# Optimization experiments

Measured on AMD Instinct MI355X. Metric: run time of the kernel, lower is better.

## Reference

```python
import jax, jax.numpy as jnp
import numpy as np

B, Q, C, H, W, E, HID_ATT, HID_MLP, NUM_CLASSES, NUM_LABELS = 8, 64, 512, 16, 16, 512, 128, 512, 14, 64


def setup_inputs() -> dict:
    key = jax.random.key(0)
    ks = jax.random.split(key, 16)
    s = 0.02
    return {
        "feature": jax.random.normal(ks[0], (B, C, H, W), jnp.float32),
        "label_ids": jax.random.randint(ks[1], (B, Q), 0, NUM_LABELS),
        "query_table": jax.random.normal(ks[2], (NUM_LABELS, E), jnp.float32) * s,
        "W_film": jax.random.normal(ks[3], (E, 2 * C), jnp.float32) * s,
        "b_film": jnp.zeros((2 * C,), jnp.float32),
        "W_att_h": jax.random.normal(ks[4], (C, HID_ATT), jnp.float32) * s,
        "b_att_h": jnp.zeros((HID_ATT,), jnp.float32),
        "W_att_f": jax.random.normal(ks[5], (HID_ATT, 1), jnp.float32) * s,
        "b_att_f": jnp.zeros((1,), jnp.float32),
        "W_mlp1": jax.random.normal(ks[6], (C, HID_MLP), jnp.float32) * s,
        "b_mlp1": jnp.zeros((HID_MLP,), jnp.float32),
        "W_mlp2": jax.random.normal(ks[7], (HID_MLP, NUM_CLASSES), jnp.float32) * s,
        "b_mlp2": jnp.zeros((NUM_CLASSES,), jnp.float32),
    }


def gelu(x):
    return jax.nn.gelu(x, approximate=False)  # torch default GELU is exact erf


def reference(feature, label_ids, query_table, W_film, b_film, W_att_h, b_att_h,
              W_att_f, b_att_f, W_mlp1, b_mlp1, W_mlp2, b_mlp2):
    # query embedding lookup: (B, Q, E)
    qe = query_table[label_ids]
    # flatten spatial: (B, HW, C)
    f = feature.reshape(feature.shape[0], feature.shape[1], -1).transpose(0, 2, 1)
    # FiLM params from queries: (B, Q, 2C) -> gamma, beta (B, Q, C)
    gb = jnp.einsum("bqe,ec->bqc", qe, W_film) + b_film
    gamma, beta = jnp.split(gb, 2, axis=-1)
    # FiLM-modulated features: (B, Q, HW, C)
    film = f[:, None, :, :] * gamma[:, :, None, :] + beta[:, :, None, :]
    # local attention MLP -> sigmoid gate (B, Q, HW, 1)
    hidden = gelu(jnp.einsum("bqnc,ch->bqnh", film, W_att_h) + b_att_h)
    attn = jax.nn.sigmoid(jnp.einsum("bqnh,ho->bqno", hidden, W_att_f) + b_att_f)
    # weighted sum pool over HW, normalized by attention mass
    pooled = (attn * film).sum(axis=2) / (attn.sum(axis=2) + 1e-8)  # (B, Q, C)
    # classification MLP
    logits = jnp.einsum("bqh,ho->bqo", gelu(jnp.einsum("bqc,ch->bqh", pooled, W_mlp1) + b_mlp1), W_mlp2) + b_mlp2
    return logits  # (B, Q, NUM_CLASSES)
```

## Files before the change

kernel.cpp:

```cpp
#include <hip/hip_runtime.h>
#include <hip/hip_bf16.h>

#define B_    8
#define Q_    64
#define C_    512
#define HW_   256
#define E_    512
#define HATT_ 128
#define HMLP_ 512
#define NCLS_ 14
#define NLAB_ 64

typedef unsigned short u16;
typedef unsigned int   u32;
typedef __attribute__((ext_vector_type(8))) short short8;
typedef __attribute__((ext_vector_type(4))) float f32x4;


__device__ __forceinline__ float gelu_fast(float x) {
    const float ax = fabsf(x);
    const float t  = __builtin_amdgcn_rcpf(1.0f + 0.3275911f * ax);
    const float p  = t * (0.254829592f +
                     t * (-0.284496736f +
                     t * (1.421413741f +
                     t * (-1.453152027f +
                     t * 1.061405429f))));
    const float e  = __expf(-x * x);
    const float er = copysignf(1.0f - p * e, x);
    return 0.5f * x * (1.0f + er);
}
__device__ __forceinline__ float sigmoid_(float x) {
    return 1.0f / (1.0f + __expf(-x));
}
__device__ __forceinline__ u16 f2bf(float x) {
    u32 u = __float_as_uint(x);
    u32 r = (u + 0x7fffu + ((u >> 16) & 1u)) >> 16;
    return (u16)r;
}
__device__ __forceinline__ float bf2f(u16 u) {
    return __uint_as_float(((u32)u) << 16);
}
__device__ __forceinline__ void gl2lds16(const void* gsrc, void* ldsdst) {
    __builtin_amdgcn_global_load_lds(
        (const __attribute__((address_space(1))) u32*)gsrc,
        (__attribute__((address_space(3))) u32*)ldsdst, 16, 0, 0);
}

__global__ __launch_bounds__(256) void prep_gbp(
    const float* __restrict__ qt, const float* __restrict__ W_film,
    float* __restrict__ GBp) {
    __shared__ float qrow[128];
    const int bid = blockIdx.x, t = threadIdx.x;
    const int l = bid >> 2, cq = bid & 3;
    if (t < 128) qrow[t] = qt[l * E_ + cq * 128 + t];
    __syncthreads();
    const float* wp = W_film + (size_t)(cq * 128) * 1024 + t * 4;
    f32x4 a = {0.f, 0.f, 0.f, 0.f};
    #pragma unroll 8
    for (int c = 0; c < 128; ++c) {
        const float4 w = *(const float4*)(wp + (size_t)c * 1024);
        const float q = qrow[c];
        a.x += q * w.x; a.y += q * w.y; a.z += q * w.z; a.w += q * w.w;
    }
    *(f32x4*)&GBp[(size_t)bid * 1024 + t * 4] = a;
}

__global__ __launch_bounds__(256) void prep_rest(
    const float* __restrict__ feature, const float* __restrict__ W_mlp1,
    const int* __restrict__ label_ids, const float* __restrict__ b_film,
    const float* __restrict__ W_att_h, const float* __restrict__ GBp,
    u16* __restrict__ W1bf, u16* __restrict__ fT,
    int* __restrict__ sperm, int* __restrict__ uled,
    int* __restrict__ ustart, int* __restrict__ nuniq,
    float* __restrict__ Gl, float* __restrict__ Bl,
    u16* __restrict__ WgT, float* __restrict__ Dlp) {

    __shared__ __align__(16) char sm[16896];
    const int bid = blockIdx.x, t = threadIdx.x;

    if (bid < 256) {
        float (*tile)[65] = (float(*)[65])sm;
        const int b = bid >> 5, c0 = ((bid >> 2) & 7) * 64, n0 = (bid & 3) * 64;
        const float* fb = feature + (size_t)b * C_ * HW_;
        const int cl = t >> 2, nq = t & 3;
        #pragma unroll
        for (int i = 0; i < 4; ++i) {
            float4 v = *(const float4*)&fb[(c0 + cl) * HW_ + n0 + nq * 16 + i * 4];
            tile[cl][nq * 16 + i * 4 + 0] = v.x;
            tile[cl][nq * 16 + i * 4 + 1] = v.y;
            tile[cl][nq * 16 + i * 4 + 2] = v.z;
            tile[cl][nq * 16 + i * 4 + 3] = v.w;
        }
        __syncthreads();
        const int nl = t >> 2, cqq = t & 3;
        u16 pk[16];
        #pragma unroll
        for (int k = 0; k < 16; ++k) pk[k] = f2bf(tile[cqq * 16 + k][nl]);
        u16* dst = fT + (size_t)(b * HW_ + n0 + nl) * C_ + c0 + cqq * 16;
        *(uint4*)dst       = *(uint4*)pk;
        *(uint4*)(dst + 8) = *(uint4*)(pk + 8);
    } else if (bid < 320) {
        const int b2 = bid - 256;
        #pragma unroll
        for (int k = 0; k < 2; ++k) {
            const int idx = (b2 * 512 + k * 256 + t) * 8;
            float4 v0 = *(const float4*)&W_mlp1[idx];
            float4 v1 = *(const float4*)&W_mlp1[idx + 4];
            u16 pk[8] = {f2bf(v0.x), f2bf(v0.y), f2bf(v0.z), f2bf(v0.w),
                         f2bf(v1.x), f2bf(v1.y), f2bf(v1.z), f2bf(v1.w)};
            *(uint4*)&W1bf[idx] = *(uint4*)pk;
        }
    } else if (bid == 320) {
        int* cnt = (int*)sm;
        int* off = cnt + 512;
        int* aux = off + 512;
        cnt[t] = 0; cnt[t + 256] = 0;
        __syncthreads();
        const int bqa = t, bqb = t + 256;
        const int ka = label_ids[bqa] * 8 + (bqa >> 6);
        const int kb = label_ids[bqb] * 8 + (bqb >> 6);
        atomicAdd(&cnt[ka], 1);
        atomicAdd(&cnt[kb], 1);
        __syncthreads();
        off[t] = cnt[t]; off[t + 256] = cnt[t + 256];
        __syncthreads();
        for (int d = 1; d < 512; d <<= 1) {
            const int i1 = t + 256;
            const int v0 = off[t]  + ((t  >= d) ? off[t  - d] : 0);
            const int v1 = off[i1] + ((i1 >= d) ? off[i1 - d] : 0);
            __syncthreads();
            off[t] = v0; off[i1] = v1;
            __syncthreads();
        }
        aux[t]       = off[t]       - cnt[t];
        aux[t + 256] = off[t + 256] - cnt[t + 256];
        __syncthreads();
        const int pa = atomicAdd(&aux[ka], 1); sperm[pa] = bqa;
        const int pb = atomicAdd(&aux[kb], 1); sperm[pb] = bqb;
        __syncthreads();
        aux[t]       = cnt[t]       ? 1 : 0;
        aux[t + 256] = cnt[t + 256] ? 1 : 0;
        __syncthreads();
        for (int d = 1; d < 512; d <<= 1) {
            const int i1 = t + 256;
            const int v0 = aux[t]  + ((t  >= d) ? aux[t  - d] : 0);
            const int v1 = aux[i1] + ((i1 >= d) ? aux[i1 - d] : 0);
            __syncthreads();
            aux[t] = v0; aux[i1] = v1;
            __syncthreads();
        }
        const int nu = aux[511];
        #pragma unroll
        for (int e = 0; e < 2; ++e) {
            const int k = t + e * 256;
            if (cnt[k]) {
                const int uidx = aux[k] - 1;
                const int st = off[k] - cnt[k];
                ustart[uidx] = st;
                uled[uidx]   = sperm[st] | ((k >> 3) << 16);
            }
        }
        if (t == 0) nuniq[0] = nu;
        for (int j = t; j <= 512; j += 256)
            if (j >= nu) ustart[j] = 512;
    } else {
        float* g_s  = (float*)sm;
        float* b_s  = g_s + 128;
        float* dred = b_s + 128;
        const int wb = bid - 321;
        const int l = wb >> 2, cq = wb & 3;

        if (t < 128) {
            const int c = cq * 128 + t;
            float g = b_film[c], be = b_film[512 + c];
            #pragma unroll
            for (int j = 0; j < 4; ++j) {
                g  += GBp[(size_t)(l * 4 + j) * 1024 + c];
                be += GBp[(size_t)(l * 4 + j) * 1024 + 512 + c];
            }
            g_s[t] = g; b_s[t] = be;
            Gl[l * C_ + c] = g;
            Bl[l * C_ + c] = be;
        }
        __syncthreads();

        const int h = t & 127, ch = t >> 7;
        const int hswz = (h >> 1) & 3;
        float dl = 0.f;
        #pragma unroll
        for (int sl = 0; sl < 2; ++sl) {
            const int ss = cq * 4 + ch * 2 + sl;
            char* dst = (char*)WgT + (size_t)l * 131072 + ss * 8192 + h * 64;
            #pragma unroll
            for (int g = 0; g < 4; ++g) {
                u16 pk[8];
                #pragma unroll
                for (int j = 0; j < 8; ++j) {
                    const int cl = ch * 64 + sl * 32 + g * 8 + j;
                    const float w = W_att_h[(size_t)(cq * 128 + cl) * HATT_ + h];
                    pk[j] = f2bf(g_s[cl] * w);
                    dl += b_s[cl] * w;
                }
                *(uint4*)(dst + ((g ^ hswz) * 16)) = *(uint4*)pk;
            }
        }
        dred[t] = dl;
        __syncthreads();
        if (t < 128)
            Dlp[(size_t)(l * 4 + cq) * 128 + t] = dred[t] + dred[128 + t];
    }
}

__global__ __launch_bounds__(256, 4) void attn_gemm(
    const float* __restrict__ W_att_f, const float* __restrict__ b_att_f,
    const float* __restrict__ b_att_h, const float* __restrict__ Dlp,
    const int*   __restrict__ uled,    const int* __restrict__ nuniq,
    const u16*   __restrict__ WgT,     const u16* __restrict__ fT,
    u16* __restrict__ pPb, float* __restrict__ pA) {

    __shared__ __align__(16) char Ash[2][8192];
    __shared__ __align__(16) char Bsh[2][8192];
    __shared__ float d_s[HATT_];
    __shared__ float wf_s[HATT_];
    __shared__ float attn_part[2][128];
    __shared__ float attn_s[128];

    const int t = threadIdx.x;
    const int idx = blockIdx.x;
    const int u = idx >> 1, nh = idx & 1;
    if (u >= nuniq[0]) return;
    const int ul = uled[u];
    const int bq = ul & 0xffff, l = ul >> 16;
    const int b = bq >> 6;

    if (t < HATT_) {
        d_s[t] = b_att_h[t]
               + Dlp[(size_t)(l * 4 + 0) * 128 + t]
               + Dlp[(size_t)(l * 4 + 1) * 128 + t]
               + Dlp[(size_t)(l * 4 + 2) * 128 + t]
               + Dlp[(size_t)(l * 4 + 3) * 128 + t];
        wf_s[t] = W_att_f[t];
    }

    const u16* fTb = fT + (size_t)b * HW_ * C_ + (size_t)nh * 128 * C_;
    const u16* Wl  = WgT + (size_t)l * 65536;

    const int an0  = t >> 2;
    const int asl0 = (t & 3) ^ ((an0 >> 1) & 3);

    #define STAGE(s_) {                                                       \
        _Pragma("unroll")                                                     \
        for (int it = 0; it < 2; ++it)                                        \
            gl2lds16(fTb + (size_t)(it * 64 + an0) * C_ + (s_) * 32           \
                         + asl0 * 8,                                          \
                     &Ash[(s_) & 1][(it * 256 + t) * 16]);                    \
        _Pragma("unroll")                                                     \
        for (int it = 0; it < 2; ++it)                                        \
            gl2lds16(Wl + (size_t)(s_) * 4096 + (size_t)(it * 256 + t) * 8,   \
                     &Bsh[(s_) & 1][(it * 256 + t) * 16]);                    \
    }

    const int lane = t & 63, w = t >> 6;
    const int wm = w >> 1, wc = w & 1;
    const int lr = lane & 15, lk = lane >> 4;

    const f32x4 zero = {0.f, 0.f, 0.f, 0.f};
    f32x4 acc[4][4];
    #pragma unroll
    for (int mi = 0; mi < 4; ++mi)
        #pragma unroll
        for (int ni = 0; ni < 4; ++ni) acc[mi][ni] = zero;

    STAGE(0);
    STAGE(1);
    asm volatile("s_waitcnt vmcnt(4)" ::: "memory");
    __builtin_amdgcn_sched_barrier(0);
    __builtin_amdgcn_s_barrier();

    #pragma unroll
    for (int s = 0; s < 16; ++s) {
        const char* Ab = Ash[s & 1];
        const char* Bb = Bsh[s & 1];
        short8 af[4], bf[4];
        #pragma unroll
        for (int mi = 0; mi < 4; ++mi) {
            const int nl = wm * 64 + mi * 16 + lr;
            af[mi] = *(const short8*)(Ab + nl * 64 + ((lk ^ ((nl >> 1) & 3)) * 16));
        }
        #pragma unroll
        for (int ni = 0; ni < 4; ++ni) {
            const int h = wc * 64 + ni * 16 + lr;
            bf[ni] = *(const short8*)(Bb + h * 64 + ((lk ^ ((h >> 1) & 3)) * 16));
        }
        asm volatile("s_waitcnt lgkmcnt(0)" ::: "memory");
        __builtin_amdgcn_sched_barrier(0);
        __builtin_amdgcn_s_barrier();
        if (s < 14) STAGE(s + 2);
        #pragma unroll
        for (int mi = 0; mi < 4; ++mi)
            #pragma unroll
            for (int ni = 0; ni < 4; ++ni)
                acc[mi][ni] = __builtin_amdgcn_mfma_f32_16x16x32_bf16(
                    af[mi], bf[ni], acc[mi][ni], 0, 0, 0);
        if (s < 15) {
            __builtin_amdgcn_sched_barrier(0);
            if (s < 14) asm volatile("s_waitcnt vmcnt(4)" ::: "memory");
            else        asm volatile("s_waitcnt vmcnt(0)" ::: "memory");
            __builtin_amdgcn_sched_barrier(0);
            __builtin_amdgcn_s_barrier();
        }
    }

    #pragma unroll
    for (int mi = 0; mi < 4; ++mi) {
        #pragma unroll
        for (int j = 0; j < 4; ++j) {
            float sum = 0.f;
            #pragma unroll
            for (int ni = 0; ni < 4; ++ni) {
                const int h = wc * 64 + ni * 16 + lr;
                sum += gelu_fast(acc[mi][ni][j] + d_s[h]) * wf_s[h];
            }
            sum += __shfl_xor(sum, 1);
            sum += __shfl_xor(sum, 2);
            sum += __shfl_xor(sum, 4);
            sum += __shfl_xor(sum, 8);
            if (lr == 0) attn_part[wc][wm * 64 + mi * 16 + lk * 4 + j] = sum;
        }
    }
    __syncthreads();
    if (t < 128)
        attn_s[t] = sigmoid_(attn_part[0][t] + attn_part[1][t] + b_att_f[0]);
    __syncthreads();
    if (t < 64) {
        float a = attn_s[t] + attn_s[t + 64];
        #pragma unroll
        for (int m = 1; m < 64; m <<= 1) a += __shfl_xor(a, m);
        if (t == 0) pA[u * 2 + nh] = a;
    }

    float* pred = (float*)Ash;
    {
        const int ng = t >> 7, cb = (t & 127) * 4;
        const u16* fp = fTb + cb;
        f32x4 p = zero;
        #pragma unroll 8
        for (int n = ng * 64; n < ng * 64 + 64; ++n) {
            const uint2 v = *(const uint2*)(fp + (size_t)n * C_);
            const float a = attn_s[n];
            p.x += a * __uint_as_float(v.x << 16);
            p.y += a * __uint_as_float(v.x & 0xffff0000u);
            p.z += a * __uint_as_float(v.y << 16);
            p.w += a * __uint_as_float(v.y & 0xffff0000u);
        }
        *(f32x4*)&pred[ng * 512 + cb] = p;
    }
    __syncthreads();
    {
        const int c0 = t * 2;
        const float v0 = pred[c0]     + pred[512 + c0];
        const float v1 = pred[c0 + 1] + pred[512 + c0 + 1];
        u16 pk[2] = {f2bf(v0), f2bf(v1)};
        *(u32*)&pPb[(size_t)(u * 2 + nh) * 512 + c0] = *(u32*)pk;
    }
}

__global__ __launch_bounds__(512) void mlp_head(
    const int*   __restrict__ uled,  const int* __restrict__ ustart,
    const int*   __restrict__ nuniq, const int* __restrict__ sperm,
    const float* __restrict__ Gl, const float* __restrict__ Bl,
    const float* __restrict__ b_mlp1, const float* __restrict__ W_mlp2,
    const float* __restrict__ b_mlp2, const u16* __restrict__ pPb,
    const float* __restrict__ pA,     const u16* __restrict__ W1bf,
    float* __restrict__ out) {

    __shared__ float pooled_s[2][C_];
    __shared__ float zred[2][2][HMLP_];
    __shared__ float z_s[2][HMLP_];
    __shared__ float red_s[32 * NCLS_];

    const int t = threadIdx.x;
    const int u0 = blockIdx.x * 2;
    const int nu = nuniq[0];
    if (u0 >= nu) return;

    {
        const int ui = t >> 8, cc = (t & 255) * 2;
        const int u = u0 + ui;
        if (u < nu) {
            const int l = uled[u] >> 16;
            const float A = pA[u * 2] + pA[u * 2 + 1];
            const float inv = 1.0f / (A + 1e-8f);
            #pragma unroll
            for (int i = 0; i < 2; ++i) {
                const int c = cc + i;
                const float p = bf2f(pPb[(size_t)(u * 2) * 512 + c])
                              + bf2f(pPb[(size_t)(u * 2 + 1) * 512 + c]);
                pooled_s[ui][c] = (Gl[l * C_ + c] * p + Bl[l * C_ + c] * A) * inv;
            }
        } else {
            pooled_s[ui][cc] = 0.f;
            pooled_s[ui][cc + 1] = 0.f;
        }
    }
    __syncthreads();

    {
        const int hp = t & 255, cg = t >> 8;
        float z00 = 0.f, z01 = 0.f, z10 = 0.f, z11 = 0.f;
        const u16* wp = W1bf + hp * 2;
        #pragma unroll 8
        for (int c = cg * 256; c < cg * 256 + 256; ++c) {
            const u32 v = *(const u32*)(wp + (size_t)c * HMLP_);
            const float w0 = __uint_as_float(v << 16);
            const float w1 = __uint_as_float(v & 0xffff0000u);
            const float pa = pooled_s[0][c], pb = pooled_s[1][c];
            z00 += pa * w0; z01 += pa * w1;
            z10 += pb * w0; z11 += pb * w1;
        }
        float2 a0 = {z00, z01}, a1 = {z10, z11};
        *(float2*)&zred[cg][0][hp * 2] = a0;
        *(float2*)&zred[cg][1][hp * 2] = a1;
    }
    __syncthreads();
    {
        const int ui = t >> 8, h2 = (t & 255) * 2;
        #pragma unroll
        for (int i = 0; i < 2; ++i) {
            const int h = h2 + i;
            z_s[ui][h] = gelu_fast(zred[0][ui][h] + zred[1][ui][h] + b_mlp1[h]);
        }
    }
    __syncthreads();

    #pragma unroll
    for (int ui = 0; ui < 2; ++ui) {
        const int u = u0 + ui;
        if (t < 448) {
            const int o = t % 14, seg = t / 14;
            float s = 0.f;
            #pragma unroll
            for (int k = 0; k < 16; ++k) {
                const int h = seg * 16 + k;
                s += z_s[ui][h] * W_mlp2[h * NCLS_ + o];
            }
            red_s[seg * NCLS_ + o] = s;
        }
        __syncthreads();
        if (u < nu && t < NCLS_) {
            float s = b_mlp2[t];
            #pragma unroll
            for (int seg = 0; seg < 32; ++seg) s += red_s[seg * NCLS_ + t];
            const int r0 = ustart[u], r1 = ustart[u + 1];
            for (int r = r0; r < r1; ++r)
                out[sperm[r] * NCLS_ + t] = s;
        }
        __syncthreads();
    }
}

extern "C" void kernel_launch(void* const* d_in, const int* in_sizes, int n_in,
                              void* d_out, int out_size, void* d_ws, size_t ws_size,
                              hipStream_t stream) {
    const float* feature   = (const float*)d_in[0];
    const int*   label_ids = (const int*)  d_in[1];
    const float* qt        = (const float*)d_in[2];
    const float* W_film    = (const float*)d_in[3];
    const float* b_film    = (const float*)d_in[4];
    const float* W_att_h   = (const float*)d_in[5];
    const float* b_att_h   = (const float*)d_in[6];
    const float* W_att_f   = (const float*)d_in[7];
    const float* b_att_f   = (const float*)d_in[8];
    const float* W_mlp1    = (const float*)d_in[9];
    const float* b_mlp1    = (const float*)d_in[10];
    const float* W_mlp2    = (const float*)d_in[11];
    const float* b_mlp2    = (const float*)d_in[12];
    float* out = (float*)d_out;

    char* wsb    = (char*)d_ws;
    float* GBp   = (float*)wsb;
    u16*   pPb   = (u16*)  wsb;
    float* pA    = (float*)(wsb + 1048576);
    int*   sperm = (int*)  (wsb + 1052672);
    int*   uled  = (int*)  (wsb + 1054720);
    int*   ustart= (int*)  (wsb + 1056768);
    int*   nuniq = (int*)  (wsb + 1060864);
    float* Dlp   = (float*)(wsb + 1064960);
    float* Gl    = (float*)(wsb + 1196032);
    float* Bl    = (float*)(wsb + 1327104);
    u16*   W1bf  = (u16*)  (wsb + 1458176);
    u16*   fTp   = (u16*)  (wsb + 1982464);
    u16*   WgT   = (u16*)  (wsb + 4079616);

    hipLaunchKernelGGL(prep_gbp, dim3(256), dim3(256), 0, stream,
                       qt, W_film, GBp);
    hipLaunchKernelGGL(prep_rest, dim3(577), dim3(256), 0, stream,
                       feature, W_mlp1, label_ids, b_film, W_att_h, GBp,
                       W1bf, fTp, sperm, uled, ustart, nuniq, Gl, Bl, WgT, Dlp);
    hipLaunchKernelGGL(attn_gemm, dim3(1024), dim3(256), 0, stream,
                       W_att_f, b_att_f, b_att_h, Dlp, uled, nuniq,
                       WgT, fTp, pPb, pA);
    hipLaunchKernelGGL(mlp_head, dim3(256), dim3(512), 0, stream,
                       uled, ustart, nuniq, sperm, Gl, Bl,
                       b_mlp1, W_mlp2, b_mlp2, pPb, pA, W1bf, out);
}
```

Measured before the change: 64.54 us.

## Fuse attention GEMM and MLP head into one kernel, one block per unique query

Merges the attention GEMM and the classification MLP head into a single kernel. Each 512-thread block now handles all 256 spatial positions of one unique (query, label) pair instead of splitting them across two blocks. This removes one kernel launch and the global round trip of the bf16 partial pooled vectors and attention sums. In exchange, the block count halves and LDS per block grows, which may reduce occupancy. The MLP head no longer shares its W_mlp1 reads across two unique queries per block.

After: 64.04 us. About the same (-0.8%).

```diff
diff --git a/kernel.cpp b/kernel.cpp
--- a/kernel.cpp
+++ b/kernel.cpp
@@ -211,23 +211,30 @@
     }
 }
 
-__global__ __launch_bounds__(256, 4) void attn_gemm(
+__global__ __launch_bounds__(512, 4) void attn_mlp(
     const float* __restrict__ W_att_f, const float* __restrict__ b_att_f,
     const float* __restrict__ b_att_h, const float* __restrict__ Dlp,
     const int*   __restrict__ uled,    const int* __restrict__ nuniq,
+    const int*   __restrict__ ustart,  const int* __restrict__ sperm,
+    const float* __restrict__ Gl,      const float* __restrict__ Bl,
+    const float* __restrict__ b_mlp1,  const float* __restrict__ W_mlp2,
+    const float* __restrict__ b_mlp2,  const u16* __restrict__ W1bf,
     const u16*   __restrict__ WgT,     const u16* __restrict__ fT,
-    u16* __restrict__ pPb, float* __restrict__ pA) {
-
-    __shared__ __align__(16) char Ash[2][8192];
+    float* __restrict__ out) {
+
+    __shared__ __align__(16) char Ash[2][16384];
     __shared__ __align__(16) char Bsh[2][8192];
     __shared__ float d_s[HATT_];
     __shared__ float wf_s[HATT_];
-    __shared__ float attn_part[2][128];
-    __shared__ float attn_s[128];
+    __shared__ float attn_part[2][HW_];
+    __shared__ float attn_s[HW_];
+    __shared__ float pooled_s[C_];
+    __shared__ float z_s[HMLP_];
+    __shared__ float red_s[32 * NCLS_];
+    __shared__ float A_sh;
 
     const int t = threadIdx.x;
-    const int idx = blockIdx.x;
-    const int u = idx >> 1, nh = idx & 1;
+    const int u = blockIdx.x;
     if (u >= nuniq[0]) return;
     const int ul = uled[u];
     const int bq = ul & 0xffff, l = ul >> 16;
@@ -242,7 +249,7 @@
         wf_s[t] = W_att_f[t];
     }
 
-    const u16* fTb = fT + (size_t)b * HW_ * C_ + (size_t)nh * 128 * C_;
+    const u16* fTb = fT + (size_t)b * HW_ * C_;
     const u16* Wl  = WgT + (size_t)l * 65536;
 
     const int an0  = t >> 2;
@@ -251,13 +258,11 @@
     #define STAGE(s_) {                                                       \
         _Pragma("unroll")                                                     \
         for (int it = 0; it < 2; ++it)                                        \
-            gl2lds16(fTb + (size_t)(it * 64 + an0) * C_ + (s_) * 32           \
+            gl2lds16(fTb + (size_t)(it * 128 + an0) * C_ + (s_) * 32          \
                          + asl0 * 8,                                          \
-                     &Ash[(s_) & 1][(it * 256 + t) * 16]);                    \
-        _Pragma("unroll")                                                     \
-        for (int it = 0; it < 2; ++it)                                        \
-            gl2lds16(Wl + (size_t)(s_) * 4096 + (size_t)(it * 256 + t) * 8,   \
-                     &Bsh[(s_) & 1][(it * 256 + t) * 16]);                    \
+                     &Ash[(s_) & 1][(it * 512 + t) * 16]);                    \
+        gl2lds16(Wl + (size_t)(s_) * 4096 + (size_t)t * 8,                    \
+                 &Bsh[(s_) & 1][t * 16]);                                     \
     }
 
     const int lane = t & 63, w = t >> 6;
@@ -273,7 +278,7 @@
 
     STAGE(0);
     STAGE(1);
-    asm volatile("s_waitcnt vmcnt(4)" ::: "memory");
+    asm volatile("s_waitcnt vmcnt(3)" ::: "memory");
     __builtin_amdgcn_sched_barrier(0);
     __builtin_amdgcn_s_barrier();
 
@@ -304,7 +309,7 @@
                     af[mi], bf[ni], acc[mi][ni], 0, 0, 0);
         if (s < 15) {
             __builtin_amdgcn_sched_barrier(0);
-            if (s < 14) asm volatile("s_waitcnt vmcnt(4)" ::: "memory");
+            if (s < 14) asm volatile("s_waitcnt vmcnt(3)" ::: "memory");
             else        asm volatile("s_waitcnt vmcnt(0)" ::: "memory");
             __builtin_amdgcn_sched_barrier(0);
             __builtin_amdgcn_s_barrier();
@@ -329,15 +334,16 @@
         }
     }
     __syncthreads();
-    if (t < 128)
+    if (t < HW_)
         attn_s[t] = sigmoid_(attn_part[0][t] + attn_part[1][t] + b_att_f[0]);
     __syncthreads();
     if (t < 64) {
-        float a = attn_s[t] + attn_s[t + 64];
+        float a = attn_s[t] + attn_s[t + 64] + attn_s[t + 128] + attn_s[t + 192];
         #pragma unroll
         for (int m = 1; m < 64; m <<= 1) a += __shfl_xor(a, m);
-        if (t == 0) pA[u * 2 + nh] = a;
-    }
+        if (t == 0) A_sh = a;
+    }
+    __syncthreads();
 
     float* pred = (float*)Ash;
     {
@@ -357,105 +363,50 @@
     }
     __syncthreads();
     {
-        const int c0 = t * 2;
-        const float v0 = pred[c0]     + pred[512 + c0];
-        const float v1 = pred[c0 + 1] + pred[512 + c0 + 1];
-        u16 pk[2] = {f2bf(v0), f2bf(v1)};
-        *(u32*)&pPb[(size_t)(u * 2 + nh) * 512 + c0] = *(u32*)pk;
-    }
-}
-
-__global__ __launch_bounds__(512) void mlp_head(
-    const int*   __restrict__ uled,  const int* __restrict__ ustart,
-    const int*   __restrict__ nuniq, const int* __restrict__ sperm,
-    const float* __restrict__ Gl, const float* __restrict__ Bl,
-    const float* __restrict__ b_mlp1, const float* __restrict__ W_mlp2,
-    const float* __restrict__ b_mlp2, const u16* __restrict__ pPb,
-    const float* __restrict__ pA,     const u16* __restrict__ W1bf,
-    float* __restrict__ out) {
-
-    __shared__ float pooled_s[2][C_];
-    __shared__ float zred[2][2][HMLP_];
-    __shared__ float z_s[2][HMLP_];
-    __shared__ float red_s[32 * NCLS_];
-
-    const int t = threadIdx.x;
-    const int u0 = blockIdx.x * 2;
-    const int nu = nuniq[0];
-    if (u0 >= nu) return;
-
-    {
-        const int ui = t >> 8, cc = (t & 255) * 2;
-        const int u = u0 + ui;
-        if (u < nu) {
-            const int l = uled[u] >> 16;
-            const float A = pA[u * 2] + pA[u * 2 + 1];
-            const float inv = 1.0f / (A + 1e-8f);
-            #pragma unroll
-            for (int i = 0; i < 2; ++i) {
-                const int c = cc + i;
-                const float p = bf2f(pPb[(size_t)(u * 2) * 512 + c])
-                              + bf2f(pPb[(size_t)(u * 2 + 1) * 512 + c]);
-                pooled_s[ui][c] = (Gl[l * C_ + c] * p + Bl[l * C_ + c] * A) * inv;
-            }
-        } else {
-            pooled_s[ui][cc] = 0.f;
-            pooled_s[ui][cc + 1] = 0.f;
-        }
-    }
-    __syncthreads();
-
+        const float A = A_sh, inv = 1.0f / (A + 1e-8f);
+        const float p = pred[t] + pred[512 + t] + pred[1024 + t] + pred[1536 + t];
+        pooled_s[t] = (Gl[(size_t)l * C_ + t] * p
+                     + Bl[(size_t)l * C_ + t] * A) * inv;
+    }
+    __syncthreads();
+
+    float* zred = (float*)Bsh;
     {
         const int hp = t & 255, cg = t >> 8;
-        float z00 = 0.f, z01 = 0.f, z10 = 0.f, z11 = 0.f;
+        float z0 = 0.f, z1 = 0.f;
         const u16* wp = W1bf + hp * 2;
         #pragma unroll 8
         for (int c = cg * 256; c < cg * 256 + 256; ++c) {
             const u32 v = *(const u32*)(wp + (size_t)c * HMLP_);
-            const float w0 = __uint_as_float(v << 16);
-            const float w1 = __uint_as_float(v & 0xffff0000u);
-            const float pa = pooled_s[0][c], pb = pooled_s[1][c];
-            z00 += pa * w0; z01 += pa * w1;
-            z10 += pb * w0; z11 += pb * w1;
-        }
-        float2 a0 = {z00, z01}, a1 = {z10, z11};
-        *(float2*)&zred[cg][0][hp * 2] = a0;
-        *(float2*)&zred[cg][1][hp * 2] = a1;
-    }
-    __syncthreads();
-    {
-        const int ui = t >> 8, h2 = (t & 255) * 2;
-        #pragma unroll
-        for (int i = 0; i < 2; ++i) {
-            const int h = h2 + i;
-            z_s[ui][h] = gelu_fast(zred[0][ui][h] + zred[1][ui][h] + b_mlp1[h]);
-        }
-    }
-    __syncthreads();
-
-    #pragma unroll
-    for (int ui = 0; ui < 2; ++ui) {
-        const int u = u0 + ui;
-        if (t < 448) {
-            const int o = t % 14, seg = t / 14;
-            float s = 0.f;
-            #pragma unroll
-            for (int k = 0; k < 16; ++k) {
-                const int h = seg * 16 + k;
-                s += z_s[ui][h] * W_mlp2[h * NCLS_ + o];
-            }
-            red_s[seg * NCLS_ + o] = s;
-        }
-        __syncthreads();
-        if (u < nu && t < NCLS_) {
-            float s = b_mlp2[t];
-            #pragma unroll
-            for (int seg = 0; seg < 32; ++seg) s += red_s[seg * NCLS_ + t];
-            const int r0 = ustart[u], r1 = ustart[u + 1];
-            for (int r = r0; r < r1; ++r)
-                out[sperm[r] * NCLS_ + t] = s;
-        }
-        __syncthreads();
+            const float pc = pooled_s[c];
+            z0 += pc * __uint_as_float(v << 16);
+            z1 += pc * __uint_as_float(v & 0xffff0000u);
+        }
+        float2 a0 = {z0, z1};
+        *(float2*)&zred[cg * 512 + hp * 2] = a0;
+    }
+    __syncthreads();
+    z_s[t] = gelu_fast(zred[t] + zred[512 + t] + b_mlp1[t]);
+    __syncthreads();
+
+    if (t < 448) {
+        const int o = t % 14, seg = t / 14;
+        float s = 0.f;
+        #pragma unroll
+        for (int k = 0; k < 16; ++k) {
+            const int h = seg * 16 + k;
+            s += z_s[h] * W_mlp2[h * NCLS_ + o];
+        }
+        red_s[seg * NCLS_ + o] = s;
+    }
+    __syncthreads();
+    if (t < NCLS_) {
+        float s = b_mlp2[t];
+        #pragma unroll
+        for (int seg = 0; seg < 32; ++seg) s += red_s[seg * NCLS_ + t];
+        const int r0 = ustart[u], r1 = ustart[u + 1];
+        for (int r = r0; r < r1; ++r)
+            out[sperm[r] * NCLS_ + t] = s;
     }
 }
 
@@ -479,28 +430,24 @@
 
     char* wsb    = (char*)d_ws;
     float* GBp   = (float*)wsb;
-    u16*   pPb   = (u16*)  wsb;
-    float* pA    = (float*)(wsb + 1048576);
-    int*   sperm = (int*)  (wsb + 1052672);
-    int*   uled  = (int*)  (wsb + 1054720);
-    int*   ustart= (int*)  (wsb + 1056768);
-    int*   nuniq = (int*)  (wsb + 1060864);
-    float* Dlp   = (float*)(wsb + 1064960);
-    float* Gl    = (float*)(wsb + 1196032);
-    float* Bl    = (float*)(wsb + 1327104);
-    u16*   W1bf  = (u16*)  (wsb + 1458176);
-    u16*   fTp   = (u16*)  (wsb + 1982464);
-    u16*   WgT   = (u16*)  (wsb + 4079616);
+    int*   sperm = (int*)  (wsb + 1048576);
+    int*   uled  = (int*)  (wsb + 1050624);
+    int*   ustart= (int*)  (wsb + 1052672);
+    int*   nuniq = (int*)  (wsb + 1056768);
+    float* Dlp   = (float*)(wsb + 1060864);
+    float* Gl    = (float*)(wsb + 1191936);
+    float* Bl    = (float*)(wsb + 1323008);
+    u16*   W1bf  = (u16*)  (wsb + 1454080);
+    u16*   fTp   = (u16*)  (wsb + 1978368);
+    u16*   WgT   = (u16*)  (wsb + 4075520);
 
     hipLaunchKernelGGL(prep_gbp, dim3(256), dim3(256), 0, stream,
                        qt, W_film, GBp);
     hipLaunchKernelGGL(prep_rest, dim3(577), dim3(256), 0, stream,
                        feature, W_mlp1, label_ids, b_film, W_att_h, GBp,
                        W1bf, fTp, sperm, uled, ustart, nuniq, Gl, Bl, WgT, Dlp);
-    hipLaunchKernelGGL(attn_gemm, dim3(1024), dim3(256), 0, stream,
+    hipLaunchKernelGGL(attn_mlp, dim3(512), dim3(512), 0, stream,
                        W_att_f, b_att_f, b_att_h, Dlp, uled, nuniq,
-                       WgT, fTp, pPb, pA);
-    hipLaunchKernelGGL(mlp_head, dim3(256), dim3(512), 0, stream,
-                       uled, ustart, nuniq, sperm, Gl, Bl,
-                       b_mlp1, W_mlp2, b_mlp2, pPb, pA, W1bf, out);
-}
+                       ustart, sperm, Gl, Bl, b_mlp1, W_mlp2, b_mlp2,
+                       W1bf, WgT, fTp, out);
+}
```
